# Optimization experiments

Hardware: AMD Instinct MI355X
Metric: run time of the kernel (lower is better)

Reference implementation:

```python
import jax, jax.numpy as jnp
import numpy as np

D_MODEL = 128
N_HEADS = 8
D_K = D_MODEL // N_HEADS
N_NODES = 50000
N_EDGES = 800000


def setup_inputs() -> dict:
    key = jax.random.key(0)
    ks = jax.random.split(key, 8)
    X = jax.random.normal(ks[0], (N_NODES, D_MODEL), dtype=jnp.float32)
    nbr_src = jax.random.randint(ks[1], (N_EDGES,), 0, N_NODES, dtype=jnp.int32)
    nbr_dst = jax.random.randint(ks[2], (N_EDGES,), 0, N_NODES, dtype=jnp.int32)
    s = 1.0 / np.sqrt(D_MODEL)
    W_qkv = jax.random.normal(ks[3], (3 * D_MODEL, D_MODEL), dtype=jnp.float32) * s
    w_bias = jax.random.normal(ks[4], (N_HEADS, D_MODEL), dtype=jnp.float32) * s
    W_gate = jax.random.normal(ks[5], (D_MODEL, D_MODEL), dtype=jnp.float32) * s
    b_gate = jax.random.normal(ks[6], (D_MODEL,), dtype=jnp.float32) * s
    W_o = jax.random.normal(ks[7], (D_MODEL, D_MODEL), dtype=jnp.float32) * s
    return {"X": X, "W_qkv": W_qkv, "w_bias": w_bias, "W_gate": W_gate,
            "b_gate": b_gate, "W_o": W_o, "nbr_src": nbr_src,
            "nbr_dst": nbr_dst, "num_cells": N_NODES}


def segment_softmax(scores, seg, num_segments):
    # scores: [E, H], seg: [E] -> softmax over edges sharing the same seg id
    mx = jax.ops.segment_max(scores, seg, num_segments=num_segments)  # [N, H]
    mx = jnp.where(jnp.isfinite(mx), mx, -1e9)
    exp_s = jnp.exp(scores - mx[seg])
    sm = jax.ops.segment_sum(exp_s, seg, num_segments=num_segments)  # [N, H]
    return exp_s / (sm[seg] + 1e-12)


def reference(X, W_qkv, w_bias, W_gate, b_gate, W_o, nbr_src, nbr_dst, num_cells):
    H, dk = N_HEADS, D_K
    scale = 1.0 / np.sqrt(dk)
    qkv = (X @ W_qkv.T).reshape(-1, 3, H, dk)      # [N, 3, H, dk]
    Q, K, V = qkv[:, 0], qkv[:, 1], qkv[:, 2]
    gate = jax.nn.sigmoid(X @ W_gate.T + b_gate).reshape(-1, H, dk)
    bias = X @ w_bias.T                             # [N, H]
    scores = jnp.einsum('ehd,ehd->eh', Q[nbr_src], K[nbr_dst]) * scale + bias[nbr_src]
    attn = segment_softmax(scores, nbr_src, num_cells)          # [E, H]
    out = jax.ops.segment_sum(attn[:, :, None] * V[nbr_dst], nbr_src,
                              num_segments=num_cells)           # [N, H, dk]
    return (gate * out).reshape(-1, D_MODEL) @ W_o.T
```

## Files before the change

### kernel.cpp

```cpp
#include <hip/hip_runtime.h>
#include <hip/hip_fp16.h>

#define DM 128
#define NHEADS 8
#define MAXDEG 64
#define SROW 136

typedef _Float16 half8 __attribute__((ext_vector_type(8)));
typedef _Float16 half2v __attribute__((ext_vector_type(2)));
typedef float floatx4 __attribute__((ext_vector_type(4)));

union H16 { half8 v8[2]; half2v h2[8]; _Float16 h[16]; };

__global__ __launch_bounds__(256) void proj_csr(
    const float* __restrict__ X, const float* __restrict__ Wqkv,
    const float* __restrict__ Wgate, const float* __restrict__ wbias,
    const float* __restrict__ b_gate,
    const int* __restrict__ nsrc, const int* __restrict__ ndst,
    int* __restrict__ cnt, int* __restrict__ csr_dst,
    _Float16* __restrict__ Q, _Float16* __restrict__ KV,
    _Float16* __restrict__ gate, float* __restrict__ bias,
    int M, int E, int P) {
  __shared__ _Float16 As[128 * SROW];
  __shared__ _Float16 Bs[64 * SROW];
  int tid = threadIdx.x;
  int bid = blockIdx.x;

  if (bid >= P) {
    int e = (bid - P) * 256 + tid;
    if (e < E) {
      int s = nsrc[e];
      int d = ndst[e];
      int p = atomicAdd(&cnt[s], 1);
      if (p < MAXDEG) csr_dst[(size_t)s * MAXDEG + p] = d;
    }
    return;
  }

  int m0 = bid * 128;

#pragma unroll
  for (int i = 0; i < 4; i++) {
    int u = tid + i * 256;
    int r = u >> 3;
    int cc = (u & 7) * 16;
    int gr = m0 + r;
    float4 f0, f1, f2, f3;
    if (gr < M) {
      const float4* src = (const float4*)(X + (size_t)gr * 128 + cc);
      f0 = src[0]; f1 = src[1]; f2 = src[2]; f3 = src[3];
    } else {
      f0 = f1 = f2 = f3 = make_float4(0.f, 0.f, 0.f, 0.f);
    }
    half8 h0 = {(_Float16)f0.x, (_Float16)f0.y, (_Float16)f0.z, (_Float16)f0.w,
                (_Float16)f1.x, (_Float16)f1.y, (_Float16)f1.z, (_Float16)f1.w};
    half8 h1 = {(_Float16)f2.x, (_Float16)f2.y, (_Float16)f2.z, (_Float16)f2.w,
                (_Float16)f3.x, (_Float16)f3.y, (_Float16)f3.z, (_Float16)f3.w};
    *(half8*)(As + r * SROW + cc) = h0;
    *(half8*)(As + r * SROW + cc + 8) = h1;
  }

  int wid = tid >> 6, lane = tid & 63;
  int quad = lane >> 4, l16 = lane & 15;
  int mw = wid * 32;

  for (int c = 0; c < 9; c++) {
    __syncthreads();
#pragma unroll
    for (int i = 0; i < 4; i++) {
      int u = tid + i * 256;
      int r = u >> 4;
      int cc = (u & 15) * 8;
      int grow = c * 64 + r;
      const float* src = nullptr;
      if (grow < 384)      src = Wqkv + (size_t)grow * 128 + cc;
      else if (grow < 512) src = Wgate + (size_t)(grow - 384) * 128 + cc;
      else if (grow < 520) src = wbias + (size_t)(grow - 512) * 128 + cc;
      half8 h = {};
      if (src) {
        float4 f0 = ((const float4*)src)[0];
        float4 f1 = ((const float4*)src)[1];
        h = half8{(_Float16)f0.x, (_Float16)f0.y, (_Float16)f0.z, (_Float16)f0.w,
                  (_Float16)f1.x, (_Float16)f1.y, (_Float16)f1.z, (_Float16)f1.w};
      }
      *(half8*)(Bs + r * SROW + cc) = h;
    }
    __syncthreads();

    floatx4 acc[2][4] = {};
#pragma unroll
    for (int kc = 0; kc < 4; kc++) {
      int ko = kc * 32 + quad * 8;
      half8 a0 = *(const half8*)(As + (mw + l16) * SROW + ko);
      half8 a1 = *(const half8*)(As + (mw + 16 + l16) * SROW + ko);
      half8 b[4];
#pragma unroll
      for (int ni = 0; ni < 4; ni++)
        b[ni] = *(const half8*)(Bs + (ni * 16 + l16) * SROW + ko);
#pragma unroll
      for (int ni = 0; ni < 4; ni++) {
        acc[0][ni] = __builtin_amdgcn_mfma_f32_16x16x32_f16(a0, b[ni], acc[0][ni], 0, 0, 0);
        acc[1][ni] = __builtin_amdgcn_mfma_f32_16x16x32_f16(a1, b[ni], acc[1][ni], 0, 0, 0);
      }
    }

    if (c == 8) {
      if (l16 < 8) {
#pragma unroll
        for (int mi = 0; mi < 2; mi++)
#pragma unroll
          for (int r = 0; r < 4; r++) {
            int row = m0 + mw + mi * 16 + quad * 4 + r;
            if (row < M) bias[(size_t)row * 8 + l16] = acc[mi][0][r];
          }
      }
    } else {
      int reg = c >> 1;
#pragma unroll
      for (int mi = 0; mi < 2; mi++) {
#pragma unroll
        for (int ni = 0; ni < 4; ni++) {
          int colL = (c & 1) * 64 + ni * 16 + l16;
#pragma unroll
          for (int r = 0; r < 4; r++) {
            int row = m0 + mw + mi * 16 + quad * 4 + r;
            if (row >= M) continue;
            float v = acc[mi][ni][r];
            if (reg == 0)      Q[(size_t)row * 128 + colL] = (_Float16)v;
            else if (reg == 1) KV[(size_t)row * 256 + colL] = (_Float16)v;
            else if (reg == 2) KV[(size_t)row * 256 + 128 + colL] = (_Float16)v;
            else gate[(size_t)row * 128 + colL] =
                   (_Float16)(1.0f / (1.0f + __expf(-(v + b_gate[colL]))));
          }
        }
      }
    }
  }
}

__global__ __launch_bounds__(1024) void attn_out(
    const int* __restrict__ cnt, const int* __restrict__ csr_dst,
    const _Float16* __restrict__ Q, const _Float16* __restrict__ KV,
    const float* __restrict__ bias, const _Float16* __restrict__ gate,
    const float* __restrict__ Wo, float* __restrict__ out, int N) {
  __shared__ _Float16 Ws[128 * SROW];
  __shared__ _Float16 Gs[16 * SROW];
  int tid = threadIdx.x;

#pragma unroll
  for (int i = 0; i < 2; i++) {
    int u = tid + i * 1024;
    int r = u >> 4;
    int cc = (u & 15) * 8;
    const float4* s = (const float4*)(Wo + (size_t)r * 128 + cc);
    float4 f0 = s[0], f1 = s[1];
    half8 h = {(_Float16)f0.x, (_Float16)f0.y, (_Float16)f0.z, (_Float16)f0.w,
               (_Float16)f1.x, (_Float16)f1.y, (_Float16)f1.z, (_Float16)f1.w};
    *(half8*)(Ws + r * SROW + cc) = h;
  }

  int wid = tid >> 6, lane = tid & 63;
  int n0 = blockIdx.x * 16;
  int n = n0 + wid;
  bool active = n < N;
  int n_eff = active ? n : 0;
  int g = lane >> 3, h = lane & 7;
  int ch0 = h * 16;

  int deg = active ? cnt[n_eff] : 0;
  if (deg > MAXDEG) deg = MAXDEG;
  int dstv = csr_dst[(size_t)n_eff * MAXDEG + lane];

  H16 qu;
  qu.v8[0] = *(const half8*)(Q + (size_t)n_eff * DM + ch0);
  qu.v8[1] = *(const half8*)(Q + (size_t)n_eff * DM + ch0 + 8);
  float bias_h = bias[(size_t)n_eff * NHEADS + h];

  float acc[16] = {};
  float den = 0.f;
  int iters = (deg + 7) >> 3;

  H16 k0, v0, k1, v1;
  k0.v8[0] = half8{}; k0.v8[1] = half8{};
  v0.v8[0] = half8{}; v0.v8[1] = half8{};
  k1 = k0; v1 = v0;
  bool b0 = false, b1 = false;
  if (0 < iters) {
    int e = g;
    b0 = e < deg;
    int d = __shfl(dstv, e);
    d = b0 ? d : 0;
    const _Float16* kvp = KV + (size_t)d * 256 + ch0;
    k0.v8[0] = *(const half8*)kvp;       k0.v8[1] = *(const half8*)(kvp + 8);
    v0.v8[0] = *(const half8*)(kvp + 128); v0.v8[1] = *(const half8*)(kvp + 136);
  }
  if (1 < iters) {
    int e = 8 + g;
    b1 = e < deg;
    int d = __shfl(dstv, e);
    d = b1 ? d : 0;
    const _Float16* kvp = KV + (size_t)d * 256 + ch0;
    k1.v8[0] = *(const half8*)kvp;       k1.v8[1] = *(const half8*)(kvp + 8);
    v1.v8[0] = *(const half8*)(kvp + 128); v1.v8[1] = *(const half8*)(kvp + 136);
  }

  for (int it = 0; it < iters; it++) {
    H16 k2, v2;
    k2.v8[0] = half8{}; k2.v8[1] = half8{};
    v2.v8[0] = half8{}; v2.v8[1] = half8{};
    bool b2 = false;
    if (it + 2 < iters) {
      int e = (it + 2) * 8 + g;
      b2 = e < deg;
      int d = __shfl(dstv, e);
      d = b2 ? d : 0;
      const _Float16* kvp = KV + (size_t)d * 256 + ch0;
      k2.v8[0] = *(const half8*)kvp;       k2.v8[1] = *(const half8*)(kvp + 8);
      v2.v8[0] = *(const half8*)(kvp + 128); v2.v8[1] = *(const half8*)(kvp + 136);
    }
    float p = 0.f;
#pragma unroll
    for (int j = 0; j < 8; j++)
      p = __builtin_amdgcn_fdot2(qu.h2[j], k0.h2[j], p, false);
    float w = __expf(p * 0.25f + bias_h);
    if (!b0) w = 0.f;
    den += w;
#pragma unroll
    for (int j = 0; j < 16; j++) acc[j] = fmaf(w, (float)v0.h[j], acc[j]);
    k0 = k1; v0 = v1; b0 = b1;
    k1 = k2; v1 = v2; b1 = b2;
  }
#pragma unroll
  for (int j = 0; j < 16; j++) {
    acc[j] += __shfl_xor(acc[j], 8);
    acc[j] += __shfl_xor(acc[j], 16);
    acc[j] += __shfl_xor(acc[j], 32);
  }
  den += __shfl_xor(den, 8);
  den += __shfl_xor(den, 16);
  den += __shfl_xor(den, 32);

  if (g == 0) {
    float inv = 1.0f / (den + 1e-12f);
    H16 gv;
    gv.v8[0] = *(const half8*)(gate + (size_t)n_eff * DM + ch0);
    gv.v8[1] = *(const half8*)(gate + (size_t)n_eff * DM + ch0 + 8);
    H16 o;
#pragma unroll
    for (int j = 0; j < 16; j++)
      o.h[j] = active ? (_Float16)(acc[j] * inv * (float)gv.h[j]) : (_Float16)0.f;
    *(half8*)(Gs + wid * SROW + ch0) = o.v8[0];
    *(half8*)(Gs + wid * SROW + ch0 + 8) = o.v8[1];
  }

  __syncthreads();

  if (wid < 8) {
    int quad = lane >> 4, l16 = lane & 15;
    floatx4 oc = {};
#pragma unroll
    for (int kc = 0; kc < 4; kc++) {
      int ko = kc * 32 + quad * 8;
      half8 a = *(const half8*)(Gs + l16 * SROW + ko);
      half8 b = *(const half8*)(Ws + (wid * 16 + l16) * SROW + ko);
      oc = __builtin_amdgcn_mfma_f32_16x16x32_f16(a, b, oc, 0, 0, 0);
    }
    int col = wid * 16 + l16;
#pragma unroll
    for (int r = 0; r < 4; r++) {
      int row = n0 + quad * 4 + r;
      if (row < N) out[(size_t)row * 128 + col] = oc[r];
    }
  }
}

extern "C" void kernel_launch(void* const* d_in, const int* in_sizes, int n_in,
                              void* d_out, int out_size, void* d_ws, size_t ws_size,
                              hipStream_t stream) {
  const float* X     = (const float*)d_in[0];
  const float* Wqkv  = (const float*)d_in[1];
  const float* wbias = (const float*)d_in[2];
  const float* Wgate = (const float*)d_in[3];
  const float* bgate = (const float*)d_in[4];
  const float* Wo    = (const float*)d_in[5];
  const int*   nsrc  = (const int*)d_in[6];
  const int*   ndst  = (const int*)d_in[7];
  int N = in_sizes[0] / 128;
  int E = in_sizes[6];
  float* out = (float*)d_out;

  char* p = (char*)d_ws;
  _Float16* Q16     = (_Float16*)p; p += (size_t)N * 128 * sizeof(_Float16);
  _Float16* KV16    = (_Float16*)p; p += (size_t)N * 256 * sizeof(_Float16);
  _Float16* gate16  = (_Float16*)p; p += (size_t)N * 128 * sizeof(_Float16);
  float* bias       = (float*)p;    p += (size_t)N * 8 * sizeof(float);
  int* cnt          = (int*)p;      p += (size_t)N * sizeof(int);
  int* csr_dst      = (int*)p;      p += (size_t)N * MAXDEG * sizeof(int);

  hipMemsetAsync(cnt, 0, (size_t)N * sizeof(int), stream);

  int P = (N + 127) / 128;
  int C = (E + 255) / 256;
  proj_csr<<<P + C, 256, 0, stream>>>(X, Wqkv, Wgate, wbias, bgate, nsrc, ndst,
                                      cnt, csr_dst, Q16, KV16, gate16, bias, N, E, P);

  attn_out<<<(N + 15) / 16, 1024, 0, stream>>>(cnt, csr_dst, Q16, KV16, bias,
                                               gate16, Wo, out, N);
}
```

Measured before the change: 240.9 us.

## Restructure attention kernel: 256-thread blocks, 8 nodes per wave, chunked Wo GEMM

The attention/output kernel moves from 1024-thread blocks (16 nodes, one per wave) to 256-thread blocks where each wave processes 8 nodes in turn, 32 nodes per block. Each lane now holds 8 channels instead of 16, with 4 edges gathered per iteration instead of 8, and the prefetch depth drops from two iterations ahead to one. The output projection converts Wo into LDS in two 64-row chunks, and every wave runs two MFMA row tiles instead of only half the waves doing work. The aim is to cut LDS use and register pressure so occupancy rises, and to spread the Wo conversion cost over more nodes. The cost is less memory-level parallelism per wave, since nodes are handled one after another with shallower prefetch.

```diff
diff --git a/kernel.cpp b/kernel.cpp
--- a/kernel.cpp
+++ b/kernel.cpp
@@ -10,7 +10,7 @@
 typedef _Float16 half2v __attribute__((ext_vector_type(2)));
 typedef float floatx4 __attribute__((ext_vector_type(4)));
 
-union H16 { half8 v8[2]; half2v h2[8]; _Float16 h[16]; };
+union H8 { half8 v; half2v h2[4]; _Float16 h[8]; };
 
 __global__ __launch_bounds__(256) void proj_csr(
     const float* __restrict__ X, const float* __restrict__ Wqkv,
@@ -138,139 +138,126 @@
   }
 }
 
-__global__ __launch_bounds__(1024) void attn_out(
+__global__ __launch_bounds__(256) void attn_out(
     const int* __restrict__ cnt, const int* __restrict__ csr_dst,
     const _Float16* __restrict__ Q, const _Float16* __restrict__ KV,
     const float* __restrict__ bias, const _Float16* __restrict__ gate,
     const float* __restrict__ Wo, float* __restrict__ out, int N) {
-  __shared__ _Float16 Ws[128 * SROW];
-  __shared__ _Float16 Gs[16 * SROW];
+  __shared__ _Float16 Ws[64 * SROW];
+  __shared__ _Float16 Gs[32 * SROW];
   int tid = threadIdx.x;
-
-#pragma unroll
-  for (int i = 0; i < 2; i++) {
-    int u = tid + i * 1024;
-    int r = u >> 4;
-    int cc = (u & 15) * 8;
-    const float4* s = (const float4*)(Wo + (size_t)r * 128 + cc);
-    float4 f0 = s[0], f1 = s[1];
-    half8 h = {(_Float16)f0.x, (_Float16)f0.y, (_Float16)f0.z, (_Float16)f0.w,
-               (_Float16)f1.x, (_Float16)f1.y, (_Float16)f1.z, (_Float16)f1.w};
-    *(half8*)(Ws + r * SROW + cc) = h;
-  }
-
   int wid = tid >> 6, lane = tid & 63;
-  int n0 = blockIdx.x * 16;
-  int n = n0 + wid;
-  bool active = n < N;
-  int n_eff = active ? n : 0;
-  int g = lane >> 3, h = lane & 7;
-  int ch0 = h * 16;
-
-  int deg = active ? cnt[n_eff] : 0;
-  if (deg > MAXDEG) deg = MAXDEG;
-  int dstv = csr_dst[(size_t)n_eff * MAXDEG + lane];
-
-  H16 qu;
-  qu.v8[0] = *(const half8*)(Q + (size_t)n_eff * DM + ch0);
-  qu.v8[1] = *(const half8*)(Q + (size_t)n_eff * DM + ch0 + 8);
-  float bias_h = bias[(size_t)n_eff * NHEADS + h];
-
-  float acc[16] = {};
-  float den = 0.f;
-  int iters = (deg + 7) >> 3;
-
-  H16 k0, v0, k1, v1;
-  k0.v8[0] = half8{}; k0.v8[1] = half8{};
-  v0.v8[0] = half8{}; v0.v8[1] = half8{};
-  k1 = k0; v1 = v0;
-  bool b0 = false, b1 = false;
-  if (0 < iters) {
-    int e = g;
-    b0 = e < deg;
-    int d = __shfl(dstv, e);
-    d = b0 ? d : 0;
-    const _Float16* kvp = KV + (size_t)d * 256 + ch0;
-    k0.v8[0] = *(const half8*)kvp;       k0.v8[1] = *(const half8*)(kvp + 8);
-    v0.v8[0] = *(const half8*)(kvp + 128); v0.v8[1] = *(const half8*)(kvp + 136);
-  }
-  if (1 < iters) {
-    int e = 8 + g;
-    b1 = e < deg;
-    int d = __shfl(dstv, e);
-    d = b1 ? d : 0;
-    const _Float16* kvp = KV + (size_t)d * 256 + ch0;
-    k1.v8[0] = *(const half8*)kvp;       k1.v8[1] = *(const half8*)(kvp + 8);
-    v1.v8[0] = *(const half8*)(kvp + 128); v1.v8[1] = *(const half8*)(kvp + 136);
-  }
-
-  for (int it = 0; it < iters; it++) {
-    H16 k2, v2;
-    k2.v8[0] = half8{}; k2.v8[1] = half8{};
-    v2.v8[0] = half8{}; v2.v8[1] = half8{};
-    bool b2 = false;
-    if (it + 2 < iters) {
-      int e = (it + 2) * 8 + g;
-      b2 = e < deg;
-      int d = __shfl(dstv, e);
-      d = b2 ? d : 0;
+  int qtr = lane >> 4, l16 = lane & 15;
+  int ch0 = l16 * 8;
+  int n0 = blockIdx.x * 32;
+
+  for (int i = 0; i < 8; i++) {
+    int slot = wid * 8 + i;
+    int n = n0 + slot;
+    bool active = n < N;
+    int n_eff = active ? n : 0;
+    int deg = active ? cnt[n_eff] : 0;
+    if (deg > MAXDEG) deg = MAXDEG;
+
+    int dstv = csr_dst[(size_t)n_eff * MAXDEG + lane];
+
+    H8 qu; qu.v = *(const half8*)(Q + (size_t)n_eff * DM + ch0);
+    float bias_h = bias[(size_t)n_eff * NHEADS + (l16 >> 1)];
+
+    float acc[8] = {};
+    float den = 0.f;
+    int iters = (deg + 3) >> 2;
+
+    H8 kc, vc; kc.v = half8{}; vc.v = half8{};
+    bool bc = false;
+    if (iters > 0) {
+      bc = qtr < deg;
+      int d = __shfl(dstv, qtr);
+      d = bc ? d : 0;
       const _Float16* kvp = KV + (size_t)d * 256 + ch0;
-      k2.v8[0] = *(const half8*)kvp;       k2.v8[1] = *(const half8*)(kvp + 8);
-      v2.v8[0] = *(const half8*)(kvp + 128); v2.v8[1] = *(const half8*)(kvp + 136);
-    }
-    float p = 0.f;
-#pragma unroll
-    for (int j = 0; j < 8; j++)
-      p = __builtin_amdgcn_fdot2(qu.h2[j], k0.h2[j], p, false);
-    float w = __expf(p * 0.25f + bias_h);
-    if (!b0) w = 0.f;
-    den += w;
-#pragma unroll
-    for (int j = 0; j < 16; j++) acc[j] = fmaf(w, (float)v0.h[j], acc[j]);
-    k0 = k1; v0 = v1; b0 = b1;
-    k1 = k2; v1 = v2; b1 = b2;
-  }
-#pragma unroll
-  for (int j = 0; j < 16; j++) {
-    acc[j] += __shfl_xor(acc[j], 8);
-    acc[j] += __shfl_xor(acc[j], 16);
-    acc[j] += __shfl_xor(acc[j], 32);
-  }
-  den += __shfl_xor(den, 8);
-  den += __shfl_xor(den, 16);
-  den += __shfl_xor(den, 32);
-
-  if (g == 0) {
-    float inv = 1.0f / (den + 1e-12f);
-    H16 gv;
-    gv.v8[0] = *(const half8*)(gate + (size_t)n_eff * DM + ch0);
-    gv.v8[1] = *(const half8*)(gate + (size_t)n_eff * DM + ch0 + 8);
-    H16 o;
-#pragma unroll
-    for (int j = 0; j < 16; j++)
-      o.h[j] = active ? (_Float16)(acc[j] * inv * (float)gv.h[j]) : (_Float16)0.f;
-    *(half8*)(Gs + wid * SROW + ch0) = o.v8[0];
-    *(half8*)(Gs + wid * SROW + ch0 + 8) = o.v8[1];
+      kc.v = *(const half8*)kvp;
+      vc.v = *(const half8*)(kvp + 128);
+    }
+    for (int it = 0; it < iters; it++) {
+      H8 kn, vn; kn.v = half8{}; vn.v = half8{};
+      bool bn = false;
+      if (it + 1 < iters) {
+        int e = (it + 1) * 4 + qtr;
+        bn = e < deg;
+        int d = __shfl(dstv, e);
+        d = bn ? d : 0;
+        const _Float16* kvp = KV + (size_t)d * 256 + ch0;
+        kn.v = *(const half8*)kvp;
+        vn.v = *(const half8*)(kvp + 128);
+      }
+      float p = 0.f;
+#pragma unroll
+      for (int j = 0; j < 4; j++)
+        p = __builtin_amdgcn_fdot2(qu.h2[j], kc.h2[j], p, false);
+      p += __shfl_xor(p, 1);
+      float w = __expf(p * 0.25f + bias_h);
+      if (!bc) w = 0.f;
+      den += w;
+#pragma unroll
+      for (int j = 0; j < 8; j++) acc[j] = fmaf(w, (float)vc.h[j], acc[j]);
+      kc = kn; vc = vn; bc = bn;
+    }
+#pragma unroll
+    for (int j = 0; j < 8; j++) {
+      acc[j] += __shfl_xor(acc[j], 16);
+      acc[j] += __shfl_xor(acc[j], 32);
+    }
+    den += __shfl_xor(den, 16);
+    den += __shfl_xor(den, 32);
+
+    if (qtr == 0) {
+      float inv = 1.0f / (den + 1e-12f);
+      H8 gv; gv.v = *(const half8*)(gate + (size_t)n_eff * DM + ch0);
+      half8 o;
+#pragma unroll
+      for (int j = 0; j < 8; j++)
+        o[j] = active ? (_Float16)(acc[j] * inv * (float)gv.h[j]) : (_Float16)0.f;
+      *(half8*)(Gs + slot * SROW + ch0) = o;
+    }
   }
 
   __syncthreads();
 
-  if (wid < 8) {
-    int quad = lane >> 4, l16 = lane & 15;
-    floatx4 oc = {};
-#pragma unroll
-    for (int kc = 0; kc < 4; kc++) {
-      int ko = kc * 32 + quad * 8;
-      half8 a = *(const half8*)(Gs + l16 * SROW + ko);
+#pragma unroll
+  for (int chunk = 0; chunk < 2; chunk++) {
+    if (chunk) __syncthreads();
+#pragma unroll
+    for (int i2 = 0; i2 < 4; i2++) {
+      int u = tid + i2 * 256;
+      int r = u >> 4;
+      int cc = (u & 15) * 8;
+      const float4* s = (const float4*)(Wo + (size_t)(chunk * 64 + r) * 128 + cc);
+      float4 f0 = s[0], f1 = s[1];
+      half8 h = {(_Float16)f0.x, (_Float16)f0.y, (_Float16)f0.z, (_Float16)f0.w,
+                 (_Float16)f1.x, (_Float16)f1.y, (_Float16)f1.z, (_Float16)f1.w};
+      *(half8*)(Ws + r * SROW + cc) = h;
+    }
+    __syncthreads();
+
+    floatx4 oc[2] = {};
+#pragma unroll
+    for (int kc2 = 0; kc2 < 4; kc2++) {
+      int ko = kc2 * 32 + qtr * 8;
       half8 b = *(const half8*)(Ws + (wid * 16 + l16) * SROW + ko);
-      oc = __builtin_amdgcn_mfma_f32_16x16x32_f16(a, b, oc, 0, 0, 0);
-    }
-    int col = wid * 16 + l16;
-#pragma unroll
-    for (int r = 0; r < 4; r++) {
-      int row = n0 + quad * 4 + r;
-      if (row < N) out[(size_t)row * 128 + col] = oc[r];
-    }
+#pragma unroll
+      for (int mi = 0; mi < 2; mi++) {
+        half8 a = *(const half8*)(Gs + (mi * 16 + l16) * SROW + ko);
+        oc[mi] = __builtin_amdgcn_mfma_f32_16x16x32_f16(a, b, oc[mi], 0, 0, 0);
+      }
+    }
+    int col = chunk * 64 + wid * 16 + l16;
+#pragma unroll
+    for (int mi = 0; mi < 2; mi++)
+#pragma unroll
+      for (int r = 0; r < 4; r++) {
+        int row = n0 + mi * 16 + qtr * 4 + r;
+        if (row < N) out[(size_t)row * 128 + col] = oc[mi][r];
+      }
   }
 }
 
@@ -304,6 +291,6 @@
   proj_csr<<<P + C, 256, 0, stream>>>(X, Wqkv, Wgate, wbias, bgate, nsrc, ndst,
                                       cnt, csr_dst, Q16, KV16, gate16, bias, N, E, P);
 
-  attn_out<<<(N + 15) / 16, 1024, 0, stream>>>(cnt, csr_dst, Q16, KV16, bias,
-                                               gate16, Wo, out, N);
+  attn_out<<<(N + 31) / 32, 256, 0, stream>>>(cnt, csr_dst, Q16, KV16, bias,
+                                              gate16, Wo, out, N);
 }
```

New measurement: 238.7 us. No clear change (-0.9%).
